# Kernel tuning notes

Measured on AMD Instinct MI355X. Metric: run time of the kernel, lower is better.

The kernel has to match this reference:

```python
import jax, jax.numpy as jnp
import numpy as np

EPS = 1e-6

def _rmsnorm(x, w):
    # Qwen3RMSNorm over last dim, computed in fp32
    var = jnp.mean(jnp.square(x), axis=-1, keepdims=True)
    return x * jax.lax.rsqrt(var + EPS) * w

def setup_inputs() -> dict:
    key = jax.random.key(0)
    ks = jax.random.split(key, 8)
    NSEQ, IN_DIM, H, G, D, SINK = 16384, 4096, 8, 4, 16, 16
    s = 0.02
    return {
        "hidden_states": jax.random.normal(ks[0], (1, NSEQ, IN_DIM), jnp.float32),
        "q_w": jax.random.normal(ks[1], (H * G * D, IN_DIM), jnp.float32) * s,
        "q_b": jax.random.normal(ks[2], (H * G * D,), jnp.float32) * s,
        "k_w": jax.random.normal(ks[3], (H * D, IN_DIM), jnp.float32) * s,
        "q_norm_w": jnp.ones((D,), jnp.float32),
        "k_norm_w": jnp.ones((D,), jnp.float32),
        "k_base": jax.random.normal(ks[4], (H, 1, SINK, D), jnp.float32) * s,
        "b": jax.random.normal(ks[5], (H, 1, G), jnp.float32) * s,
    }

def reference(hidden_states, q_w, q_b, k_w, q_norm_w, k_norm_w, k_base, b):
    H, _, SINK, D = k_base.shape
    G = b.shape[-1]
    d = jnp.sqrt(jnp.asarray(D, hidden_states.dtype))
    h = hidden_states[0]                                   # [n, in_dim]
    n = h.shape[0]
    # projections + RMSNorm
    q = _rmsnorm((h @ q_w.T + q_b).reshape(n, H, G, D), q_norm_w)   # [n,H,G,D]
    k = _rmsnorm((h @ k_w.T).reshape(n, H, D), k_norm_w)            # [n,H,D]
    # logit: per-token key against its own group queries + learned bias
    logit = jnp.einsum('nhd,nhgd->hng', k, q) / d + b               # [H,n,G]
    # logit_base: learned sink keys against queries
    logit_base = jnp.einsum('hsd,nhgd->hnsg', k_base[:, 0], q) / d  # [H,n,S,G]
    # sigmoid-difference gate, summed over sink tokens
    denom = 1.0 + jnp.sum(jnp.exp(logit_base - logit[:, :, None, :]), axis=2)  # [H,n,G]
    score = jnp.mean(1.0 / denom, axis=-1)                          # [H,n]
    return score[None]                                              # [1,H,n]
```

## Files before the change

kernel.cpp:

```cpp
#include <hip/hip_runtime.h>
#include <hip/hip_bf16.h>

typedef __attribute__((ext_vector_type(8))) short bf16x8;
typedef __attribute__((ext_vector_type(4))) float f32x4;
typedef unsigned short u16;

constexpr int NSEQ = 16384;
constexpr int KD   = 4096;
constexpr int NQ   = 512;
constexpr int NCOL = 640;
constexpr int BM   = 128;
constexpr int BK   = 32;
constexpr int KHALF = 2048;
constexpr int NKS  = KHALF / BK;
constexpr int CHUNKS_PER_TILE = NCOL * BK * 2 / 16;
constexpr int NTILES = KD / BK;
constexpr int TOTAL_CHUNKS = CHUNKS_PER_TILE * NTILES;
constexpr int TILE_U16 = CHUNKS_PER_TILE * 8;
constexpr int BUF_BYTES = 49152;

__device__ __forceinline__ unsigned bf_round(float x) {
    unsigned u = __builtin_bit_cast(unsigned, x);
    unsigned r = u + 0x7FFFu + ((u >> 16) & 1u);
    return r >> 16;
}
__device__ __forceinline__ unsigned pk2(float lo, float hi) {
    return bf_round(lo) | (bf_round(hi) << 16);
}
__device__ __forceinline__ float bfu(unsigned u) {
    return __builtin_bit_cast(float, u << 16);
}

__global__ __launch_bounds__(256) void wconv_kernel(
    const float* __restrict__ qw, const float* __restrict__ kw,
    u16* __restrict__ Wst)
{
    int cg = blockIdx.x * 256 + threadIdx.x;
    int kk = cg / CHUNKS_PER_TILE;
    int c  = cg - kk * CHUNKS_PER_TILE;
    int n  = c >> 2;
    int s  = c & 3;
    int k0 = kk * BK + ((s ^ (n & 3)) << 3);
    const float* src = (n < NQ) ? (qw + (size_t)n * KD + k0)
                                : (kw + (size_t)(n - NQ) * KD + k0);
    float4 v0 = *(const float4*)(src);
    float4 v1 = *(const float4*)(src + 4);
    int4 o;
    o.x = (int)pk2(v0.x, v0.y);
    o.y = (int)pk2(v0.z, v0.w);
    o.z = (int)pk2(v1.x, v1.y);
    o.w = (int)pk2(v1.z, v1.w);
    *(int4*)(Wst + (size_t)cg * 8) = o;
}

__global__ __launch_bounds__(512, 2) void gemm_kernel(
    const float* __restrict__ hid, const u16* __restrict__ Wst,
    u16* __restrict__ P0, u16* __restrict__ P1)
{
    __shared__ char smem[2 * BUF_BYTES];

    const int t    = threadIdx.x;
    const int lane = t & 63;
    const int wid  = t >> 6;
    const int wm   = wid >> 2;
    const int wq   = wid & 3;
    const int mblk = blockIdx.x & 127;
    const int kh   = blockIdx.x >> 7;
    const int row0 = mblk * BM;

    const float* hk   = hid + (size_t)row0 * KD + kh * KHALF;
    const u16*  wbase = Wst + (size_t)(kh * NKS) * TILE_U16;
    u16* P = kh ? P1 : P0;

    f32x4 acc[4][10] = {};

    const int ar  = t >> 2;
    const int ks8 = t & 3;
    const float* gA = hk + (size_t)ar * KD + ks8 * 8;
    const int aWoff = ar * 64 + ((ks8 * 16) ^ ((ar & 3) << 4));

    const int bn    = lane & 15;
    const int kslot = lane >> 4;
    const int koff  = (kslot * 16) ^ ((bn & 3) << 4);

    float4 vA0a, vA0b, vA1a, vA1b;

    vA0a = *(const float4*)(gA);
    vA0b = *(const float4*)(gA + 4);
    vA1a = *(const float4*)(gA + BK);
    vA1b = *(const float4*)(gA + BK + 4);
    {
        const u16* tile = wbase;
        #pragma unroll
        for (int it = 0; it < 5; ++it)
            __builtin_amdgcn_global_load_lds(
                (const __attribute__((address_space(1))) void*)(tile + (size_t)(it * 512 + t) * 8),
                (__attribute__((address_space(3))) void*)(smem + wid * 1024 + it * 8192),
                16, 0, 0);
    }
    {
        int4 ap;
        ap.x = (int)pk2(vA0a.x, vA0a.y);
        ap.y = (int)pk2(vA0a.z, vA0a.w);
        ap.z = (int)pk2(vA0b.x, vA0b.y);
        ap.w = (int)pk2(vA0b.z, vA0b.w);
        *(int4*)(smem + 40960 + aWoff) = ap;
    }
    asm volatile("s_waitcnt lgkmcnt(0)" ::: "memory");
    __builtin_amdgcn_s_barrier();

#define GSTEP(tt, VAWa, VAWb, VALa, VALb)                                        \
    do {                                                                         \
        const int cur_ = (tt) & 1;                                               \
        char* sBc = smem + cur_ * BUF_BYTES;                                     \
        char* sAc = sBc + 40960;                                                 \
        if ((tt) < NKS - 1) {                                                    \
            char* sBn = smem + (cur_ ^ 1) * BUF_BYTES;                           \
            const u16* tile = wbase + (size_t)((tt) + 1) * TILE_U16;             \
            _Pragma("unroll")                                                    \
            for (int it = 0; it < 5; ++it)                                       \
                __builtin_amdgcn_global_load_lds(                                \
                    (const __attribute__((address_space(1))) void*)(tile + (size_t)(it * 512 + t) * 8), \
                    (__attribute__((address_space(3))) void*)(sBn + wid * 1024 + it * 8192), \
                    16, 0, 0);                                                   \
            {                                                                    \
                int4 ap;                                                         \
                ap.x = (int)pk2(VAWa.x, VAWa.y);                                 \
                ap.y = (int)pk2(VAWa.z, VAWa.w);                                 \
                ap.z = (int)pk2(VAWb.x, VAWb.y);                                 \
                ap.w = (int)pk2(VAWb.z, VAWb.w);                                 \
                *(int4*)(sBn + 40960 + aWoff) = ap;                              \
            }                                                                    \
            if ((tt) < NKS - 2) {                                                \
                VALa = *(const float4*)(gA + ((tt) + 2) * BK);                   \
                VALb = *(const float4*)(gA + ((tt) + 2) * BK + 4);               \
                asm volatile("s_waitcnt vmcnt(7)" ::: "memory");                 \
            } else {                                                             \
                asm volatile("s_waitcnt vmcnt(5)" ::: "memory");                 \
            }                                                                    \
        } else {                                                                 \
            asm volatile("s_waitcnt vmcnt(0)" ::: "memory");                     \
        }                                                                        \
        bf16x8 af[4];                                                            \
        _Pragma("unroll")                                                        \
        for (int m = 0; m < 4; ++m)                                              \
            af[m] = *(const bf16x8*)(sAc + (wm * 64 + m * 16 + bn) * 64 + koff); \
        _Pragma("unroll")                                                        \
        for (int f = 0; f < 10; ++f) {                                           \
            bf16x8 bfr = *(const bf16x8*)(sBc + (wq * 160 + f * 16 + bn) * 64 + koff); \
            _Pragma("unroll")                                                    \
            for (int m = 0; m < 4; ++m)                                          \
                acc[m][f] = __builtin_amdgcn_mfma_f32_16x16x32_bf16(af[m], bfr, acc[m][f], 0, 0, 0); \
        }                                                                        \
        if ((tt) < NKS - 1) {                                                    \
            asm volatile("s_waitcnt lgkmcnt(0)" ::: "memory");                   \
            __builtin_amdgcn_s_barrier();                                        \
        }                                                                        \
    } while (0)

    for (int t2 = 0; t2 < NKS / 2; ++t2) {
        const int tt = 2 * t2;
        GSTEP(tt,     vA1a, vA1b, vA0a, vA0b);
        GSTEP(tt + 1, vA0a, vA0b, vA1a, vA1b);
    }
#undef GSTEP

    const int crow = (lane >> 4) << 2;
    const int ccol = lane & 15;
    u16* Pp = P + (size_t)(row0 + wm * 64) * NCOL + wq * 160 + ccol;
    #pragma unroll
    for (int m = 0; m < 4; ++m)
        #pragma unroll
        for (int f = 0; f < 10; ++f)
            #pragma unroll
            for (int j = 0; j < 4; ++j)
                Pp[(size_t)(m * 16 + crow + j) * NCOL + f * 16] =
                    (u16)bf_round(acc[m][f][j]);
}

__global__ __launch_bounds__(256) void gate_kernel(
    const u16* __restrict__ P0, const u16* __restrict__ P1,
    const float* __restrict__ qb,
    const float* __restrict__ qnw, const float* __restrict__ knw,
    const float* __restrict__ kbase, const float* __restrict__ bb,
    float* __restrict__ out)
{
    __shared__ float skb[8 * 16 * 16];
    __shared__ float sqb[512];
    __shared__ float sb[32];
    __shared__ float snw[32];

    int tid = threadIdx.x;
    for (int i = tid; i < 2048; i += 256) skb[i] = kbase[i];
    for (int i = tid; i < 512;  i += 256) sqb[i] = qb[i];
    if (tid < 32) sb[tid] = bb[tid];
    if (tid < 16) snw[tid] = qnw[tid];
    else if (tid < 32) snw[tid] = knw[tid - 16];
    __syncthreads();

    int gid = blockIdx.x * 256 + tid;
    int tok = gid >> 5;
    int hh  = (gid >> 2) & 7;
    int g   = gid & 3;

    const u16* r0 = P0 + (size_t)tok * NCOL;
    const u16* r1 = P1 + (size_t)tok * NCOL;
    const int qoff = (hh * 4 + g) * 16;

    float q[16];
    float ss = 0.f;
    {
        int4 a0 = *(const int4*)(r0 + qoff);
        int4 a1 = *(const int4*)(r0 + qoff + 8);
        int4 b0 = *(const int4*)(r1 + qoff);
        int4 b1 = *(const int4*)(r1 + qoff + 8);
        const int* aw = (const int*)&a0;
        int wa[8] = {a0.x, a0.y, a0.z, a0.w, a1.x, a1.y, a1.z, a1.w};
        int wb[8] = {b0.x, b0.y, b0.z, b0.w, b1.x, b1.y, b1.z, b1.w};
        (void)aw;
        #pragma unroll
        for (int i = 0; i < 8; ++i) {
            unsigned ua = (unsigned)wa[i], ub = (unsigned)wb[i];
            q[2*i+0] = bfu(ua & 0xFFFFu) + bfu(ub & 0xFFFFu) + sqb[qoff + 2*i+0];
            q[2*i+1] = bfu(ua >> 16)     + bfu(ub >> 16)     + sqb[qoff + 2*i+1];
        }
        #pragma unroll
        for (int d = 0; d < 16; ++d) ss += q[d] * q[d];
    }
    float rq = rsqrtf(ss * (1.f / 16.f) + 1e-6f);
    #pragma unroll
    for (int d = 0; d < 16; ++d) q[d] *= rq * snw[d];

    float k[16];
    float sk = 0.f;
    {
        const int koffb = NQ + hh * 16;
        int4 a0 = *(const int4*)(r0 + koffb);
        int4 a1 = *(const int4*)(r0 + koffb + 8);
        int4 b0 = *(const int4*)(r1 + koffb);
        int4 b1 = *(const int4*)(r1 + koffb + 8);
        int wa[8] = {a0.x, a0.y, a0.z, a0.w, a1.x, a1.y, a1.z, a1.w};
        int wb[8] = {b0.x, b0.y, b0.z, b0.w, b1.x, b1.y, b1.z, b1.w};
        #pragma unroll
        for (int i = 0; i < 8; ++i) {
            unsigned ua = (unsigned)wa[i], ub = (unsigned)wb[i];
            k[2*i+0] = bfu(ua & 0xFFFFu) + bfu(ub & 0xFFFFu);
            k[2*i+1] = bfu(ua >> 16)     + bfu(ub >> 16);
        }
        #pragma unroll
        for (int d = 0; d < 16; ++d) sk += k[d] * k[d];
    }
    float rk = rsqrtf(sk * (1.f / 16.f) + 1e-6f);

    float logit = 0.f;
    #pragma unroll
    for (int d = 0; d < 16; ++d) logit += (k[d] * rk * snw[16 + d]) * q[d];
    logit = logit * 0.25f + sb[hh * 4 + g];

    float accum = 0.f;
    const float* kbh = skb + hh * 256;
    #pragma unroll
    for (int s = 0; s < 16; ++s) {
        float lb = 0.f;
        #pragma unroll
        for (int d = 0; d < 16; ++d) lb += kbh[s * 16 + d] * q[d];
        accum += __expf(lb * 0.25f - logit);
    }
    float r = 1.f / (1.f + accum);

    r += __shfl_xor(r, 1);
    r += __shfl_xor(r, 2);
    if (g == 0) out[(size_t)hh * NSEQ + tok] = r * 0.25f;
}

extern "C" void kernel_launch(void* const* d_in, const int* in_sizes, int n_in,
                              void* d_out, int out_size, void* d_ws, size_t ws_size,
                              hipStream_t stream)
{
    const float* hid = (const float*)d_in[0];
    const float* qw  = (const float*)d_in[1];
    const float* qb  = (const float*)d_in[2];
    const float* kw  = (const float*)d_in[3];
    const float* qnw = (const float*)d_in[4];
    const float* knw = (const float*)d_in[5];
    const float* kb  = (const float*)d_in[6];
    const float* bb  = (const float*)d_in[7];
    float* out = (float*)d_out;

    u16* Wst = (u16*)d_ws;
    u16* P0  = (u16*)((char*)d_ws + (size_t)NCOL * KD * 2);
    u16* P1  = P0 + (size_t)NSEQ * NCOL;

    wconv_kernel<<<TOTAL_CHUNKS / 256, 256, 0, stream>>>(qw, kw, Wst);
    gemm_kernel<<<256, 512, 0, stream>>>(hid, Wst, P0, P1);
    gate_kernel<<<NSEQ * 32 / 256, 256, 0, stream>>>(P0, P1, qb, qnw, knw, kb, bb, out);
}
```

Baseline: 186.8 us.

## Triple-buffer GEMM LDS pipeline, change swizzle, remap blocks across XCDs

Moves the split-K bf16 GEMM from a double-buffered to a triple-buffered LDS pipeline. Global A loads are prefetched three tiles ahead and B tiles two ahead, with matching vmcnt waits. The LDS XOR swizzle now keys on (row>>1)&3 instead of row&3, and the weight pre-conversion kernel is changed to match; the intent is fewer bank conflicts on the bf16x8 reads. Block indices are remapped so that the two K-halves and neighbouring M-blocks land on chosen XCDs, aiming for better L2 reuse. The extra buffer raises LDS use to about 144KB per block, which may allow only one block per CU instead of the two requested by launch bounds.

```diff
diff --git a/kernel.cpp b/kernel.cpp
--- a/kernel.cpp
+++ b/kernel.cpp
@@ -17,6 +17,7 @@
 constexpr int NTILES = KD / BK;
 constexpr int TOTAL_CHUNKS = CHUNKS_PER_TILE * NTILES;
 constexpr int TILE_U16 = CHUNKS_PER_TILE * 8;
+constexpr int B_BYTES  = 40960;
 constexpr int BUF_BYTES = 49152;
 
 __device__ __forceinline__ unsigned bf_round(float x) {
@@ -40,7 +41,7 @@
     int c  = cg - kk * CHUNKS_PER_TILE;
     int n  = c >> 2;
     int s  = c & 3;
-    int k0 = kk * BK + ((s ^ (n & 3)) << 3);
+    int k0 = kk * BK + ((s ^ ((n >> 1) & 3)) << 3);
     const float* src = (n < NQ) ? (qw + (size_t)n * KD + k0)
                                 : (kw + (size_t)(n - NQ) * KD + k0);
     float4 v0 = *(const float4*)(src);
@@ -57,15 +58,18 @@
     const float* __restrict__ hid, const u16* __restrict__ Wst,
     u16* __restrict__ P0, u16* __restrict__ P1)
 {
-    __shared__ char smem[2 * BUF_BYTES];
+    __shared__ __align__(16) char smem[3 * BUF_BYTES];
 
     const int t    = threadIdx.x;
     const int lane = t & 63;
     const int wid  = t >> 6;
     const int wm   = wid >> 2;
     const int wq   = wid & 3;
-    const int mblk = blockIdx.x & 127;
-    const int kh   = blockIdx.x >> 7;
+
+    const int b    = blockIdx.x;
+    const int xcd  = b & 7;
+    const int kh   = xcd & 1;
+    const int mblk = (b >> 3) * 4 + (xcd >> 1);
     const int row0 = mblk * BM;
 
     const float* hk   = hid + (size_t)row0 * KD + kh * KHALF;
@@ -77,93 +81,119 @@
     const int ar  = t >> 2;
     const int ks8 = t & 3;
     const float* gA = hk + (size_t)ar * KD + ks8 * 8;
-    const int aWoff = ar * 64 + ((ks8 * 16) ^ ((ar & 3) << 4));
+    const int aWoff = ar * 64 + ((ks8 ^ ((ar >> 1) & 3)) << 4);
 
     const int bn    = lane & 15;
     const int kslot = lane >> 4;
-    const int koff  = (kslot * 16) ^ ((bn & 3) << 4);
-
-    float4 vA0a, vA0b, vA1a, vA1b;
-
-    vA0a = *(const float4*)(gA);
-    vA0b = *(const float4*)(gA + 4);
-    vA1a = *(const float4*)(gA + BK);
-    vA1b = *(const float4*)(gA + BK + 4);
-    {
-        const u16* tile = wbase;
-        #pragma unroll
-        for (int it = 0; it < 5; ++it)
-            __builtin_amdgcn_global_load_lds(
-                (const __attribute__((address_space(1))) void*)(tile + (size_t)(it * 512 + t) * 8),
-                (__attribute__((address_space(3))) void*)(smem + wid * 1024 + it * 8192),
-                16, 0, 0);
-    }
-    {
-        int4 ap;
-        ap.x = (int)pk2(vA0a.x, vA0a.y);
-        ap.y = (int)pk2(vA0a.z, vA0a.w);
-        ap.z = (int)pk2(vA0b.x, vA0b.y);
-        ap.w = (int)pk2(vA0b.z, vA0b.w);
-        *(int4*)(smem + 40960 + aWoff) = ap;
-    }
-    asm volatile("s_waitcnt lgkmcnt(0)" ::: "memory");
-    __builtin_amdgcn_s_barrier();
-
-#define GSTEP(tt, VAWa, VAWb, VALa, VALb)                                        \
-    do {                                                                         \
-        const int cur_ = (tt) & 1;                                               \
-        char* sBc = smem + cur_ * BUF_BYTES;                                     \
-        char* sAc = sBc + 40960;                                                 \
-        if ((tt) < NKS - 1) {                                                    \
-            char* sBn = smem + (cur_ ^ 1) * BUF_BYTES;                           \
-            const u16* tile = wbase + (size_t)((tt) + 1) * TILE_U16;             \
-            _Pragma("unroll")                                                    \
-            for (int it = 0; it < 5; ++it)                                       \
-                __builtin_amdgcn_global_load_lds(                                \
-                    (const __attribute__((address_space(1))) void*)(tile + (size_t)(it * 512 + t) * 8), \
-                    (__attribute__((address_space(3))) void*)(sBn + wid * 1024 + it * 8192), \
-                    16, 0, 0);                                                   \
-            {                                                                    \
-                int4 ap;                                                         \
-                ap.x = (int)pk2(VAWa.x, VAWa.y);                                 \
-                ap.y = (int)pk2(VAWa.z, VAWa.w);                                 \
-                ap.z = (int)pk2(VAWb.x, VAWb.y);                                 \
-                ap.w = (int)pk2(VAWb.z, VAWb.w);                                 \
-                *(int4*)(sBn + 40960 + aWoff) = ap;                              \
-            }                                                                    \
-            if ((tt) < NKS - 2) {                                                \
-                VALa = *(const float4*)(gA + ((tt) + 2) * BK);                   \
-                VALb = *(const float4*)(gA + ((tt) + 2) * BK + 4);               \
-                asm volatile("s_waitcnt vmcnt(7)" ::: "memory");                 \
-            } else {                                                             \
-                asm volatile("s_waitcnt vmcnt(5)" ::: "memory");                 \
-            }                                                                    \
-        } else {                                                                 \
-            asm volatile("s_waitcnt vmcnt(0)" ::: "memory");                     \
-        }                                                                        \
-        bf16x8 af[4];                                                            \
+    const int koff  = (kslot ^ ((bn >> 1) & 3)) << 4;
+
+    float4 s0a, s0b, s1a, s1b, s2a, s2b;
+
+#define GLDS(X, BW)                                                              \
+    do {                                                                         \
+        char* sBn_ = smem + (BW) * BUF_BYTES;                                    \
+        const u16* tile_ = wbase + (size_t)(X) * TILE_U16;                       \
+        _Pragma("unroll")                                                        \
+        for (int it = 0; it < 5; ++it)                                           \
+            __builtin_amdgcn_global_load_lds(                                    \
+                (const __attribute__((address_space(1))) void*)(tile_ + (size_t)(it * 512 + t) * 8), \
+                (__attribute__((address_space(3))) void*)(sBn_ + wid * 1024 + it * 8192), \
+                16, 0, 0);                                                       \
+    } while (0)
+
+#define DSWA(BW, Ra, Rb)                                                         \
+    do {                                                                         \
+        int4 ap_;                                                                \
+        ap_.x = (int)pk2(Ra.x, Ra.y);                                            \
+        ap_.y = (int)pk2(Ra.z, Ra.w);                                            \
+        ap_.z = (int)pk2(Rb.x, Rb.y);                                            \
+        ap_.w = (int)pk2(Rb.z, Rb.w);                                            \
+        *(int4*)(smem + (BW) * BUF_BYTES + B_BYTES + aWoff) = ap_;               \
+    } while (0)
+
+#define COMPUTE(BC)                                                              \
+    do {                                                                         \
+        char* sBc_ = smem + (BC) * BUF_BYTES;                                    \
+        char* sAc_ = sBc_ + B_BYTES;                                             \
+        bf16x8 af_[4];                                                           \
         _Pragma("unroll")                                                        \
         for (int m = 0; m < 4; ++m)                                              \
-            af[m] = *(const bf16x8*)(sAc + (wm * 64 + m * 16 + bn) * 64 + koff); \
+            af_[m] = *(const bf16x8*)(sAc_ + (wm * 64 + m * 16 + bn) * 64 + koff); \
         _Pragma("unroll")                                                        \
         for (int f = 0; f < 10; ++f) {                                           \
-            bf16x8 bfr = *(const bf16x8*)(sBc + (wq * 160 + f * 16 + bn) * 64 + koff); \
+            bf16x8 bfr_ = *(const bf16x8*)(sBc_ + (wq * 160 + f * 16 + bn) * 64 + koff); \
             _Pragma("unroll")                                                    \
             for (int m = 0; m < 4; ++m)                                          \
-                acc[m][f] = __builtin_amdgcn_mfma_f32_16x16x32_bf16(af[m], bfr, acc[m][f], 0, 0, 0); \
+                acc[m][f] = __builtin_amdgcn_mfma_f32_16x16x32_bf16(af_[m], bfr_, acc[m][f], 0, 0, 0); \
         }                                                                        \
-        if ((tt) < NKS - 1) {                                                    \
-            asm volatile("s_waitcnt lgkmcnt(0)" ::: "memory");                   \
-            __builtin_amdgcn_s_barrier();                                        \
-        }                                                                        \
-    } while (0)
-
-    for (int t2 = 0; t2 < NKS / 2; ++t2) {
-        const int tt = 2 * t2;
-        GSTEP(tt,     vA1a, vA1b, vA0a, vA0b);
-        GSTEP(tt + 1, vA0a, vA0b, vA1a, vA1b);
+    } while (0)
+
+#define ALOAD(X, Ra, Rb)                                                         \
+    do {                                                                         \
+        Ra = *(const float4*)(gA + (X) * BK);                                    \
+        Rb = *(const float4*)(gA + (X) * BK + 4);                                \
+    } while (0)
+
+#define BARR()                                                                   \
+    do {                                                                         \
+        asm volatile("s_waitcnt lgkmcnt(0)" ::: "memory");                       \
+        __builtin_amdgcn_s_barrier();                                            \
+    } while (0)
+
+    ALOAD(0, s0a, s0b);
+    ALOAD(1, s1a, s1b);
+    ALOAD(2, s2a, s2b);
+    GLDS(0, 0);
+    DSWA(0, s0a, s0b);
+    ALOAD(3, s0a, s0b);
+    GLDS(1, 1);
+    DSWA(1, s1a, s1b);
+    BARR();
+
+#pragma unroll 1
+    for (int t3 = 0; t3 < 20; ++t3) {
+        const int tt = t3 * 3;
+        ALOAD(tt + 4, s1a, s1b);
+        GLDS(tt + 2, 2);
+        DSWA(2, s2a, s2b);
+        asm volatile("s_waitcnt vmcnt(14)" ::: "memory");
+        COMPUTE(0);
+        BARR();
+        ALOAD(tt + 5, s2a, s2b);
+        GLDS(tt + 3, 0);
+        DSWA(0, s0a, s0b);
+        asm volatile("s_waitcnt vmcnt(14)" ::: "memory");
+        COMPUTE(1);
+        BARR();
+        ALOAD(tt + 6, s0a, s0b);
+        GLDS(tt + 4, 1);
+        DSWA(1, s1a, s1b);
+        asm volatile("s_waitcnt vmcnt(14)" ::: "memory");
+        COMPUTE(2);
+        BARR();
     }
-#undef GSTEP
+
+    GLDS(62, 2);
+    DSWA(2, s2a, s2b);
+    asm volatile("s_waitcnt vmcnt(12)" ::: "memory");
+    COMPUTE(0);
+    BARR();
+    GLDS(63, 0);
+    DSWA(0, s0a, s0b);
+    asm volatile("s_waitcnt vmcnt(10)" ::: "memory");
+    COMPUTE(1);
+    BARR();
+    asm volatile("s_waitcnt vmcnt(5)" ::: "memory");
+    COMPUTE(2);
+    BARR();
+    asm volatile("s_waitcnt vmcnt(0)" ::: "memory");
+    COMPUTE(0);
+
+#undef GLDS
+#undef DSWA
+#undef COMPUTE
+#undef ALOAD
+#undef BARR
 
     const int crow = (lane >> 4) << 2;
     const int ccol = lane & 15;
@@ -214,10 +244,8 @@
         int4 a1 = *(const int4*)(r0 + qoff + 8);
         int4 b0 = *(const int4*)(r1 + qoff);
         int4 b1 = *(const int4*)(r1 + qoff + 8);
-        const int* aw = (const int*)&a0;
         int wa[8] = {a0.x, a0.y, a0.z, a0.w, a1.x, a1.y, a1.z, a1.w};
         int wb[8] = {b0.x, b0.y, b0.z, b0.w, b1.x, b1.y, b1.z, b1.w};
-        (void)aw;
         #pragma unroll
         for (int i = 0; i < 8; ++i) {
             unsigned ua = (unsigned)wa[i], ub = (unsigned)wb[i];
```

New measurement: 175.5 us. 6.1% less time.

## Interleave GEMM loads with MFMA phases, retune LDS swizzle and XCD block mapping

Applied to the files above, without the earlier changes.

The GEMM main loop becomes four phases per K-step. Each phase issues a slice of the next tile's global-to-LDS loads and the A-tile conversion, then runs its MFMAs under raised wave priority, with barriers between phases. The LDS XOR swizzle now keys on (row>>1)&3 instead of row&3, intended to cut bank conflicts for 16-byte reads. Blocks are also remapped so the two K-halves of neighbouring M blocks land on chosen XCDs for cache locality. The cost is more barriers per step, and the vmcnt(0) wait at the end of each step may expose load latency.

```diff
diff --git a/kernel.cpp b/kernel.cpp
--- a/kernel.cpp
+++ b/kernel.cpp
@@ -17,6 +17,7 @@
 constexpr int NTILES = KD / BK;
 constexpr int TOTAL_CHUNKS = CHUNKS_PER_TILE * NTILES;
 constexpr int TILE_U16 = CHUNKS_PER_TILE * 8;
+constexpr int B_BYTES  = 40960;
 constexpr int BUF_BYTES = 49152;
 
 __device__ __forceinline__ unsigned bf_round(float x) {
@@ -40,7 +41,7 @@
     int c  = cg - kk * CHUNKS_PER_TILE;
     int n  = c >> 2;
     int s  = c & 3;
-    int k0 = kk * BK + ((s ^ (n & 3)) << 3);
+    int k0 = kk * BK + ((s ^ ((n >> 1) & 3)) << 3);
     const float* src = (n < NQ) ? (qw + (size_t)n * KD + k0)
                                 : (kw + (size_t)(n - NQ) * KD + k0);
     float4 v0 = *(const float4*)(src);
@@ -57,15 +58,18 @@
     const float* __restrict__ hid, const u16* __restrict__ Wst,
     u16* __restrict__ P0, u16* __restrict__ P1)
 {
-    __shared__ char smem[2 * BUF_BYTES];
+    __shared__ __align__(16) char smem[2 * BUF_BYTES];
 
     const int t    = threadIdx.x;
     const int lane = t & 63;
     const int wid  = t >> 6;
     const int wm   = wid >> 2;
     const int wq   = wid & 3;
-    const int mblk = blockIdx.x & 127;
-    const int kh   = blockIdx.x >> 7;
+
+    const int b    = blockIdx.x;
+    const int xcd  = b & 7;
+    const int kh   = xcd & 1;
+    const int mblk = (b >> 3) * 4 + (xcd >> 1);
     const int row0 = mblk * BM;
 
     const float* hk   = hid + (size_t)row0 * KD + kh * KHALF;
@@ -77,93 +81,124 @@
     const int ar  = t >> 2;
     const int ks8 = t & 3;
     const float* gA = hk + (size_t)ar * KD + ks8 * 8;
-    const int aWoff = ar * 64 + ((ks8 * 16) ^ ((ar & 3) << 4));
+    const int aWoff = ar * 64 + ((ks8 ^ ((ar >> 1) & 3)) << 4);
 
     const int bn    = lane & 15;
     const int kslot = lane >> 4;
-    const int koff  = (kslot * 16) ^ ((bn & 3) << 4);
-
-    float4 vA0a, vA0b, vA1a, vA1b;
-
-    vA0a = *(const float4*)(gA);
-    vA0b = *(const float4*)(gA + 4);
-    vA1a = *(const float4*)(gA + BK);
-    vA1b = *(const float4*)(gA + BK + 4);
-    {
-        const u16* tile = wbase;
-        #pragma unroll
-        for (int it = 0; it < 5; ++it)
-            __builtin_amdgcn_global_load_lds(
-                (const __attribute__((address_space(1))) void*)(tile + (size_t)(it * 512 + t) * 8),
-                (__attribute__((address_space(3))) void*)(smem + wid * 1024 + it * 8192),
-                16, 0, 0);
-    }
-    {
-        int4 ap;
-        ap.x = (int)pk2(vA0a.x, vA0a.y);
-        ap.y = (int)pk2(vA0a.z, vA0a.w);
-        ap.z = (int)pk2(vA0b.x, vA0b.y);
-        ap.w = (int)pk2(vA0b.z, vA0b.w);
-        *(int4*)(smem + 40960 + aWoff) = ap;
-    }
-    asm volatile("s_waitcnt lgkmcnt(0)" ::: "memory");
-    __builtin_amdgcn_s_barrier();
-
-#define GSTEP(tt, VAWa, VAWb, VALa, VALb)                                        \
-    do {                                                                         \
-        const int cur_ = (tt) & 1;                                               \
-        char* sBc = smem + cur_ * BUF_BYTES;                                     \
-        char* sAc = sBc + 40960;                                                 \
-        if ((tt) < NKS - 1) {                                                    \
-            char* sBn = smem + (cur_ ^ 1) * BUF_BYTES;                           \
-            const u16* tile = wbase + (size_t)((tt) + 1) * TILE_U16;             \
-            _Pragma("unroll")                                                    \
-            for (int it = 0; it < 5; ++it)                                       \
-                __builtin_amdgcn_global_load_lds(                                \
-                    (const __attribute__((address_space(1))) void*)(tile + (size_t)(it * 512 + t) * 8), \
-                    (__attribute__((address_space(3))) void*)(sBn + wid * 1024 + it * 8192), \
-                    16, 0, 0);                                                   \
-            {                                                                    \
-                int4 ap;                                                         \
-                ap.x = (int)pk2(VAWa.x, VAWa.y);                                 \
-                ap.y = (int)pk2(VAWa.z, VAWa.w);                                 \
-                ap.z = (int)pk2(VAWb.x, VAWb.y);                                 \
-                ap.w = (int)pk2(VAWb.z, VAWb.w);                                 \
-                *(int4*)(sBn + 40960 + aWoff) = ap;                              \
+    const int koff  = (kslot ^ ((bn >> 1) & 3)) << 4;
+
+    float4 s0a, s0b, s1a, s1b;
+
+#define GL(IT, TP, SBN)                                                          \
+    __builtin_amdgcn_global_load_lds(                                            \
+        (const __attribute__((address_space(1))) void*)((TP) + (size_t)((IT) * 512 + t) * 8), \
+        (__attribute__((address_space(3))) void*)((SBN) + wid * 1024 + (IT) * 8192), \
+        16, 0, 0)
+
+#define BAR1()                                                                   \
+    __builtin_amdgcn_s_barrier();                                                \
+    asm volatile("s_waitcnt lgkmcnt(0)" ::: "memory");                           \
+    __builtin_amdgcn_sched_barrier(0);                                           \
+    __builtin_amdgcn_s_setprio(1)
+
+#define ENDP()                                                                   \
+    __builtin_amdgcn_sched_barrier(0);                                           \
+    __builtin_amdgcn_s_setprio(0);                                               \
+    __builtin_amdgcn_s_barrier()
+
+#define RDA(M) (*(const bf16x8*)(sAc + (wm * 64 + (M) * 16 + bn) * 64 + koff))
+#define RDB(F) (*(const bf16x8*)(sBc + (wq * 160 + (F) * 16 + bn) * 64 + koff))
+
+#define MF(F, B)                                                                 \
+    acc[0][F] = __builtin_amdgcn_mfma_f32_16x16x32_bf16(af0, B, acc[0][F], 0, 0, 0); \
+    acc[1][F] = __builtin_amdgcn_mfma_f32_16x16x32_bf16(af1, B, acc[1][F], 0, 0, 0); \
+    acc[2][F] = __builtin_amdgcn_mfma_f32_16x16x32_bf16(af2, B, acc[2][F], 0, 0, 0); \
+    acc[3][F] = __builtin_amdgcn_mfma_f32_16x16x32_bf16(af3, B, acc[3][F], 0, 0, 0)
+
+#define STEP(TT, CUR, SWa, SWb, SLa, SLb, HG, HA)                                \
+    {                                                                            \
+        char* sBc = smem + (CUR) * BUF_BYTES;                                    \
+        char* sAc = sBc + B_BYTES;                                               \
+        char* sBn = smem + ((CUR) ^ 1) * BUF_BYTES;                              \
+        const u16* tp = wbase + (size_t)((TT) + 1) * TILE_U16;                   \
+                  \
+        bf16x8 af0 = RDA(0), af1 = RDA(1), af2 = RDA(2), af3 = RDA(3);           \
+        {                                                                        \
+            bf16x8 b0 = RDB(0), b1 = RDB(1);                                     \
+            if (HA) { SLa = *(const float4*)(gA + ((TT) + 2) * BK);              \
+                      SLb = *(const float4*)(gA + ((TT) + 2) * BK + 4); }        \
+            if (HG) { GL(0, tp, sBn); GL(1, tp, sBn); }                          \
+            BAR1();                                                              \
+            MF(0, b0); MF(1, b1);                                                \
+            ENDP();                                                              \
+        }                                                                        \
+                         \
+        {                                                                        \
+            bf16x8 b0 = RDB(2), b1 = RDB(3), b2 = RDB(4);                        \
+            if (HG) {                                                            \
+                int4 ap_;                                                        \
+                ap_.x = (int)pk2(SWa.x, SWa.y);  ap_.y = (int)pk2(SWa.z, SWa.w); \
+                ap_.z = (int)pk2(SWb.x, SWb.y);  ap_.w = (int)pk2(SWb.z, SWb.w); \
+                *(int4*)(sBn + B_BYTES + aWoff) = ap_;                           \
+                GL(2, tp, sBn); GL(3, tp, sBn);                                  \
             }                                                                    \
-            if ((tt) < NKS - 2) {                                                \
-                VALa = *(const float4*)(gA + ((tt) + 2) * BK);                   \
-                VALb = *(const float4*)(gA + ((tt) + 2) * BK + 4);               \
-                asm volatile("s_waitcnt vmcnt(7)" ::: "memory");                 \
-            } else {                                                             \
-                asm volatile("s_waitcnt vmcnt(5)" ::: "memory");                 \
-            }                                                                    \
-        } else {                                                                 \
-            asm volatile("s_waitcnt vmcnt(0)" ::: "memory");                     \
+            BAR1();                                                              \
+            MF(2, b0); MF(3, b1); MF(4, b2);                                     \
+            ENDP();                                                              \
         }                                                                        \
-        bf16x8 af[4];                                                            \
-        _Pragma("unroll")                                                        \
-        for (int m = 0; m < 4; ++m)                                              \
-            af[m] = *(const bf16x8*)(sAc + (wm * 64 + m * 16 + bn) * 64 + koff); \
-        _Pragma("unroll")                                                        \
-        for (int f = 0; f < 10; ++f) {                                           \
-            bf16x8 bfr = *(const bf16x8*)(sBc + (wq * 160 + f * 16 + bn) * 64 + koff); \
-            _Pragma("unroll")                                                    \
-            for (int m = 0; m < 4; ++m)                                          \
-                acc[m][f] = __builtin_amdgcn_mfma_f32_16x16x32_bf16(af[m], bfr, acc[m][f], 0, 0, 0); \
+                                             \
+        {                                                                        \
+            bf16x8 b0 = RDB(5), b1 = RDB(6), b2 = RDB(7);                        \
+            if (HG) GL(4, tp, sBn);                                              \
+            BAR1();                                                              \
+            MF(5, b0); MF(6, b1); MF(7, b2);                                     \
+            ENDP();                                                              \
         }                                                                        \
-        if ((tt) < NKS - 1) {                                                    \
-            asm volatile("s_waitcnt lgkmcnt(0)" ::: "memory");                   \
+                           \
+        {                                                                        \
+            bf16x8 b0 = RDB(8), b1 = RDB(9);                                     \
+            BAR1();                                                              \
+            MF(8, b0); MF(9, b1);                                                \
+            __builtin_amdgcn_sched_barrier(0);                                   \
+            __builtin_amdgcn_s_setprio(0);                                       \
+            if (HG) { asm volatile("s_waitcnt vmcnt(0)" ::: "memory"); }         \
             __builtin_amdgcn_s_barrier();                                        \
         }                                                                        \
-    } while (0)
-
-    for (int t2 = 0; t2 < NKS / 2; ++t2) {
-        const int tt = 2 * t2;
-        GSTEP(tt,     vA1a, vA1b, vA0a, vA0b);
-        GSTEP(tt + 1, vA0a, vA0b, vA1a, vA1b);
-    }
-#undef GSTEP
+    }
+
+    s0a = *(const float4*)(gA);
+    s0b = *(const float4*)(gA + 4);
+    {
+        const u16* tp = wbase;
+        GL(0, tp, smem); GL(1, tp, smem); GL(2, tp, smem); GL(3, tp, smem); GL(4, tp, smem);
+    }
+    s1a = *(const float4*)(gA + BK);
+    s1b = *(const float4*)(gA + BK + 4);
+    {
+        int4 ap_;
+        ap_.x = (int)pk2(s0a.x, s0a.y);  ap_.y = (int)pk2(s0a.z, s0a.w);
+        ap_.z = (int)pk2(s0b.x, s0b.y);  ap_.w = (int)pk2(s0b.z, s0b.w);
+        *(int4*)(smem + B_BYTES + aWoff) = ap_;
+    }
+    asm volatile("s_waitcnt vmcnt(0) lgkmcnt(0)" ::: "memory");
+    __builtin_amdgcn_s_barrier();
+
+#pragma unroll 1
+    for (int t2 = 0; t2 < 31; ++t2) {
+        const int tt = t2 * 2;
+        STEP(tt,     0, s1a, s1b, s0a, s0b, 1, 1)
+        STEP(tt + 1, 1, s0a, s0b, s1a, s1b, 1, 1)
+    }
+    STEP(62, 0, s1a, s1b, s0a, s0b, 1, 0)
+    STEP(63, 1, s0a, s0b, s1a, s1b, 0, 0)
+
+#undef GL
+#undef BAR1
+#undef ENDP
+#undef RDA
+#undef RDB
+#undef MF
+#undef STEP
 
     const int crow = (lane >> 4) << 2;
     const int ccol = lane & 15;
@@ -214,10 +249,8 @@
         int4 a1 = *(const int4*)(r0 + qoff + 8);
         int4 b0 = *(const int4*)(r1 + qoff);
         int4 b1 = *(const int4*)(r1 + qoff + 8);
-        const int* aw = (const int*)&a0;
         int wa[8] = {a0.x, a0.y, a0.z, a0.w, a1.x, a1.y, a1.z, a1.w};
         int wb[8] = {b0.x, b0.y, b0.z, b0.w, b1.x, b1.y, b1.z, b1.w};
-        (void)aw;
         #pragma unroll
         for (int i = 0; i < 8; ++i) {
             unsigned ua = (unsigned)wa[i], ub = (unsigned)wb[i];
```

Result: slower. 193.4 us (+3.5%).
